# Kernel tuning notes

Hardware: AMD Instinct MI355X
Metric: run time of the kernel (lower is better)

Reference implementation:

```python
import jax, jax.numpy as jnp
import numpy as np

B, N, C = 2, 1024, 256
HEADS, DH = 8, 32
INNER = HEADS * DH
L, P = 3, 9
FF = 512
DEPTH = 2
KNN_K = (16, 64)
SHAPES_NP = np.array([[128, 128], [64, 64], [32, 32]], np.int32)
LEN = int((SHAPES_NP[:, 0] * SHAPES_NP[:, 1]).sum())


def _ln(x, g, b, eps=1e-5):
    m = x.mean(-1, keepdims=True)
    v = ((x - m) ** 2).mean(-1, keepdims=True)
    return (x - m) * jax.lax.rsqrt(v + eps) * g + b


def _knn_gather(x, pos, k):
    # pos: [B,N,3]; self-KNN (includes self as nearest)
    sq = jnp.sum(pos ** 2, -1)
    d2 = sq[:, :, None] + sq[:, None, :] - 2.0 * jnp.einsum('bnd,bmd->bnm', pos, pos)
    _, idx = jax.lax.top_k(-d2, k)  # [B,N,k]
    return jax.vmap(lambda xb, ib: xb[ib])(x, idx)  # [B,N,k,C]


def _self_attn_knn(x, pos3d, Wq, Wkv, Wo, bo, k):
    Bq, Nq, _ = x.shape
    knn_x = _knn_gather(x, pos3d, k)
    q = (x @ Wq).reshape(Bq, Nq, HEADS, DH)
    kk, vv = jnp.split(knn_x @ Wkv, 2, -1)
    kk = kk.reshape(Bq, Nq, k, HEADS, DH)
    vv = vv.reshape(Bq, Nq, k, HEADS, DH)
    attn = jax.nn.softmax(jnp.einsum('bnhd,bnshd->bnhs', q, kk) * (DH ** -0.5), -1)
    out = jnp.einsum('bnhs,bnshd->bnhd', attn, vv).reshape(Bq, Nq, INNER)
    return out @ Wo + bo


def _bilinear(value_l, loc, Hl, Wl):
    # value_l: [B, Hl*Wl, HEADS, DH]; loc: [B,N,HEADS,P,2] normalized [0,1]
    # grid_sample(align_corners=False, padding_mode='zeros') semantics
    Bq, Nq, Hh, Pp, _ = loc.shape
    xf = loc[..., 0] * Wl - 0.5
    yf = loc[..., 1] * Hl - 0.5
    x0 = jnp.floor(xf)
    y0 = jnp.floor(yf)
    out = jnp.zeros((Bq, Nq, Hh, Pp, DH), value_l.dtype)
    for dy in (0.0, 1.0):
        for dx in (0.0, 1.0):
            ix, iy = x0 + dx, y0 + dy
            w = (1.0 - jnp.abs(xf - ix)) * (1.0 - jnp.abs(yf - iy))
            valid = (ix >= 0) & (ix <= Wl - 1) & (iy >= 0) & (iy <= Hl - 1)
            flat = (jnp.clip(iy, 0, Hl - 1) * Wl + jnp.clip(ix, 0, Wl - 1)).astype(jnp.int32)
            flat = flat.transpose(0, 1, 3, 2).reshape(Bq, Nq * Pp, Hh)
            idx = jnp.broadcast_to(flat[..., None], (Bq, Nq * Pp, Hh, DH))
            g = jnp.take_along_axis(value_l, idx, axis=1)
            g = g.reshape(Bq, Nq, Pp, Hh, DH).transpose(0, 1, 3, 2, 4)
            out = out + g * (w * valid)[..., None]
    return out


def _msdeform(q, ref, value_src, Wval, bval, Woff, boff, Waw, baw, Wo, bo):
    Bq, Nq, _ = q.shape
    value = (value_src @ Wval + bval).reshape(Bq, -1, HEADS, DH)
    off = (q @ Woff + boff).reshape(Bq, Nq, HEADS, L, P, 2)
    aw = jax.nn.softmax((q @ Waw + baw).reshape(Bq, Nq, HEADS, L * P), -1)
    aw = aw.reshape(Bq, Nq, HEADS, L, P)
    normalizer = jnp.asarray(SHAPES_NP[:, ::-1].copy(), jnp.float32)  # (W,H) per level
    loc = ref[:, :, None, :, None, :] + off / normalizer[None, None, None, :, None, :]
    out = jnp.zeros((Bq, Nq, HEADS, DH), q.dtype)
    start = 0
    for l in range(L):
        Hl, Wl = int(SHAPES_NP[l, 0]), int(SHAPES_NP[l, 1])
        v_l = value[:, start:start + Hl * Wl]
        samp = _bilinear(v_l, loc[:, :, :, l], Hl, Wl)  # [B,N,H,P,DH]
        out = out + jnp.einsum('bnhpd,bnhp->bnhd', samp, aw[:, :, :, l])
        start += Hl * Wl
    return out.reshape(Bq, Nq, INNER) @ Wo + bo


def _forward(x, src, center_pos, center_pos3d, W_pos, b_pos, ln1_g, ln1_b, ln2_g, ln2_b, ln3_g, ln3_b,
             Wq, Wkv, Wo_sa, bo_sa, Wval, bval, Woff, boff, Waw, baw, Wo_ca, bo_ca, W1, b1, W2, b2):
    cpe = center_pos[..., 0, :] @ W_pos + b_pos  # pos_embedding(center_pos[...,0,:])
    ref = center_pos  # [B,N,L,2]
    for i in range(DEPTH):
        h = _ln(x + cpe, ln1_g[i], ln1_b[i])
        x = x + _self_attn_knn(h, center_pos3d, Wq[i], Wkv[i], Wo_sa[i], bo_sa[i], KNN_K[i])
        q = _ln(x, ln2_g[i], ln2_b[i]) + cpe  # with_pos_embed(norm(x), query_pos)
        s = _ln(src, ln2_g[i], ln2_b[i])      # PreNorm applies same LN to src
        x = x + _msdeform(q, ref, s, Wval[i], bval[i], Woff[i], boff[i], Waw[i], baw[i], Wo_ca[i], bo_ca[i])
        hf = _ln(x, ln3_g[i], ln3_b[i])
        x = x + (jax.nn.gelu(hf @ W1[i] + b1[i], approximate=False) @ W2[i] + b2[i])
    return x


def setup_inputs():
    key = jax.random.key(0)
    ks = iter(jax.random.split(key, 64))
    rn = lambda shape, s=1.0: jax.random.normal(next(ks), shape, jnp.float32) * s
    w = 0.02
    starts = np.concatenate([[0], np.cumsum(SHAPES_NP[:, 0] * SHAPES_NP[:, 1])[:-1]]).astype(np.int32)
    return {
        'x': rn((B, N, C)),
        'src': rn((B, LEN, C)),
        'center_pos': jax.random.uniform(next(ks), (B, N, L, 2), jnp.float32),
        'center_pos3d': rn((B, N, 3)),
        'spatial_shapes': jnp.asarray(SHAPES_NP),
        'level_start_index': jnp.asarray(starts),
        'W_pos': rn((2, C), w), 'b_pos': jnp.zeros((C,), jnp.float32),
        'ln1_g': jnp.ones((DEPTH, C)), 'ln1_b': jnp.zeros((DEPTH, C)),
        'ln2_g': jnp.ones((DEPTH, C)), 'ln2_b': jnp.zeros((DEPTH, C)),
        'ln3_g': jnp.ones((DEPTH, C)), 'ln3_b': jnp.zeros((DEPTH, C)),
        'Wq': rn((DEPTH, C, INNER), w), 'Wkv': rn((DEPTH, C, 2 * INNER), w),
        'Wo_sa': rn((DEPTH, INNER, C), w), 'bo_sa': jnp.zeros((DEPTH, C)),
        'Wval': rn((DEPTH, C, INNER), w), 'bval': jnp.zeros((DEPTH, INNER)),
        'Woff': rn((DEPTH, C, HEADS * L * P * 2), w), 'boff': rn((DEPTH, HEADS * L * P * 2), w),
        'Waw': rn((DEPTH, C, HEADS * L * P), w), 'baw': jnp.zeros((DEPTH, HEADS * L * P)),
        'Wo_ca': rn((DEPTH, INNER, C), w), 'bo_ca': jnp.zeros((DEPTH, C)),
        'W1': rn((DEPTH, C, FF), w), 'b1': jnp.zeros((DEPTH, FF)),
        'W2': rn((DEPTH, FF, C), w), 'b2': jnp.zeros((DEPTH, C)),
    }


def reference(x, src, center_pos, center_pos3d, spatial_shapes, level_start_index, W_pos, b_pos,
              ln1_g, ln1_b, ln2_g, ln2_b, ln3_g, ln3_b, Wq, Wkv, Wo_sa, bo_sa,
              Wval, bval, Woff, boff, Waw, baw, Wo_ca, bo_ca, W1, b1, W2, b2):
    # spatial_shapes / level_start_index are fixed constants (SHAPES_NP) baked into the level loop.
    return _forward(x, src, center_pos, center_pos3d, W_pos, b_pos, ln1_g, ln1_b, ln2_g, ln2_b,
                    ln3_g, ln3_b, Wq, Wkv, Wo_sa, bo_sa, Wval, bval, Woff, boff, Waw, baw,
                    Wo_ca, bo_ca, W1, b1, W2, b2)
```

## Files before the change

kernel.cpp:

```cpp
#include <hip/hip_runtime.h>
#include <math.h>


#define DEV __device__ __forceinline__

typedef __attribute__((ext_vector_type(8))) short bf16x8;
typedef __attribute__((ext_vector_type(4))) float floatx4;

DEV float gelu_f(float v) { return 0.5f * v * (1.0f + erff(v * 0.7071067811865475f)); }

DEV unsigned short f2bf(float f) {
    unsigned u = __float_as_uint(f);
    return (unsigned short)((u + 0x7fffu + ((u >> 16) & 1u)) >> 16);
}

__global__ __launch_bounds__(256) void k_lnsrc(const float* __restrict__ x, unsigned short* __restrict__ out) {
    int wid = threadIdx.x >> 6, lane = threadIdx.x & 63;
    size_t row = (size_t)blockIdx.x * 4 + wid;
    float4 v = ((const float4*)(x + row * 256))[lane];
    float s = (v.x + v.y) + (v.z + v.w);
#pragma unroll
    for (int o = 32; o; o >>= 1) s += __shfl_xor(s, o);
    float mean = s * (1.0f / 256.0f);
    float dx = v.x - mean, dy = v.y - mean, dz = v.z - mean, dw = v.w - mean;
    float q = (dx * dx + dy * dy) + (dz * dz + dw * dw);
#pragma unroll
    for (int o = 32; o; o >>= 1) q += __shfl_xor(q, o);
    float rstd = 1.0f / sqrtf(q * (1.0f / 256.0f) + 1e-5f);
    ushort4 o4;
    o4.x = f2bf(dx * rstd);
    o4.y = f2bf(dy * rstd);
    o4.z = f2bf(dz * rstd);
    o4.w = f2bf(dw * rstd);
    ((ushort4*)(out + row * 256))[lane] = o4;
}

__global__ __launch_bounds__(256) void k_lnfused(const float* __restrict__ x, const float* pre, const float* post,
                                                 const float* __restrict__ g, const float* __restrict__ b,
                                                 unsigned short* __restrict__ out) {
    int wid = threadIdx.x >> 6, lane = threadIdx.x & 63;
    size_t row = (size_t)blockIdx.x * 4 + wid;
    float4 v = ((const float4*)(x + row * 256))[lane];
    if (pre) {
        float4 p = ((const float4*)(pre + row * 256))[lane];
        v.x += p.x; v.y += p.y; v.z += p.z; v.w += p.w;
    }
    float s = (v.x + v.y) + (v.z + v.w);
#pragma unroll
    for (int o = 32; o; o >>= 1) s += __shfl_xor(s, o);
    float mean = s * (1.0f / 256.0f);
    float dx = v.x - mean, dy = v.y - mean, dz = v.z - mean, dw = v.w - mean;
    float q = (dx * dx + dy * dy) + (dz * dz + dw * dw);
#pragma unroll
    for (int o = 32; o; o >>= 1) q += __shfl_xor(q, o);
    float rstd = 1.0f / sqrtf(q * (1.0f / 256.0f) + 1e-5f);
    float4 gg = ((const float4*)g)[lane], bb = ((const float4*)b)[lane];
    float4 o4;
    o4.x = dx * rstd * gg.x + bb.x;
    o4.y = dy * rstd * gg.y + bb.y;
    o4.z = dz * rstd * gg.z + bb.z;
    o4.w = dw * rstd * gg.w + bb.w;
    if (post) {
        float4 p = ((const float4*)(post + row * 256))[lane];
        o4.x += p.x; o4.y += p.y; o4.z += p.z; o4.w += p.w;
    }
    ushort4 u4;
    u4.x = f2bf(o4.x); u4.y = f2bf(o4.y); u4.z = f2bf(o4.z); u4.w = f2bf(o4.w);
    ((ushort4*)(out + row * 256))[lane] = u4;
}

__global__ __launch_bounds__(256) void k_cpe(const float* __restrict__ cpos, const float* __restrict__ Wp,
                                             const float* __restrict__ bp, float* __restrict__ cpe) {
    int bn = blockIdx.x, c = threadIdx.x;
    float px = cpos[(size_t)bn * 6 + 0], py = cpos[(size_t)bn * 6 + 1];
    cpe[(size_t)bn * 256 + c] = px * Wp[c] + py * Wp[256 + c] + bp[c];
}

__global__ __launch_bounds__(256) void k_knn2(const float* __restrict__ pos, int* __restrict__ k16,
                                              int* __restrict__ k64) {
    __shared__ float sp[3072];
    int b = blockIdx.x >> 8;
    int n0 = (blockIdx.x & 255) * 4;
    for (int t = threadIdx.x; t < 3072; t += 256) sp[t] = pos[(size_t)b * 3072 + t];
    __syncthreads();
    int wid = threadIdx.x >> 6, lane = threadIdx.x & 63;
    int n = n0 + wid;
    float qx = sp[n * 3], qy = sp[n * 3 + 1], qz = sp[n * 3 + 2];
    float sqn = (qx * qx + qy * qy) + qz * qz;
    unsigned du[16];
#pragma unroll
    for (int t = 0; t < 16; t++) {
        int m = t * 64 + lane;
        float mx = sp[m * 3], my = sp[m * 3 + 1], mz = sp[m * 3 + 2];
        float sqm = (mx * mx + my * my) + mz * mz;
        float dt = (qx * mx + qy * my) + qz * mz;
        float d2 = (sqn + sqm) - 2.0f * dt;
        unsigned u = __float_as_uint(d2);
        du[t] = (u & 0x80000000u) ? ~u : (u | 0x80000000u);
    }
    unsigned long long lmask = (1ull << lane) - 1ull;

    auto cnt_le = [&](unsigned p) {
        int c = 0;
#pragma unroll
        for (int t = 0; t < 16; t++) c += __popcll(__ballot(du[t] <= p));
        return c;
    };
    auto find_T = [&](int K) {
        unsigned lo = 0u, hi = 0xFFFFFFFFu;
        while (lo < hi) {
            unsigned mid = lo + ((hi - lo) >> 1);
            if (cnt_le(mid) >= K) hi = mid; else lo = mid + 1;
        }
        return hi;
    };
    auto emit = [&](int K, unsigned T, int* out) {
        int base = 0;
#pragma unroll
        for (int t = 0; t < 16; t++) {
            bool lt = du[t] < T;
            unsigned long long mk = __ballot(lt);
            if (lt) out[base + __popcll(mk & lmask)] = t * 64 + lane;
            base += __popcll(mk);
        }
        int need = K - base, eb = 0;
#pragma unroll
        for (int t = 0; t < 16; t++) {
            bool eq = du[t] == T;
            unsigned long long mk = __ballot(eq);
            if (eq) {
                int r = eb + __popcll(mk & lmask);
                if (r < need) out[base + r] = t * 64 + lane;
            }
            eb += __popcll(mk);
        }
    };
    unsigned T16 = find_T(16);
    emit(16, T16, k16 + ((size_t)b * 1024 + n) * 16);
    unsigned T64 = find_T(64);
    emit(64, T64, k64 + ((size_t)b * 1024 + n) * 64);
}

template <int KK>
__global__ __launch_bounds__(256) void k_attn(const float* __restrict__ hqkv, const int* __restrict__ kidx,
                                              unsigned short* __restrict__ out) {
    int bn = blockIdx.x;
    int b = bn >> 10;
    int tid = threadIdx.x;
    __shared__ float sq[256];
    __shared__ float sa[8][KK];
    __shared__ int si[KK];
    if (tid < KK) si[tid] = kidx[(size_t)bn * KK + tid];
    sq[tid] = hqkv[(size_t)bn * 768 + tid] * 0.17677669529663689f;
    __syncthreads();
    const float* kvb = hqkv + (size_t)b * 1024 * 768;
#pragma unroll
    for (int pair = tid; pair < 8 * KK; pair += 256) {
        int s = pair & (KK - 1);
        int h = pair / KK;
        const float4* kr = (const float4*)(kvb + (size_t)si[s] * 768 + 256 + h * 32);
        const float4* q4 = (const float4*)&sq[h * 32];
        float a0 = 0.f, a1 = 0.f, a2 = 0.f, a3 = 0.f;
#pragma unroll
        for (int e = 0; e < 8; e++) {
            float4 kv = kr[e];
            float4 qv = q4[e];
            a0 = fmaf(kv.x, qv.x, a0);
            a1 = fmaf(kv.y, qv.y, a1);
            a2 = fmaf(kv.z, qv.z, a2);
            a3 = fmaf(kv.w, qv.w, a3);
        }
        sa[h][s] = (a0 + a1) + (a2 + a3);
    }
    __syncthreads();
    int h = tid >> 5, d = tid & 31;
    float mx = -1e30f;
    for (int s = d; s < KK; s += 32) mx = fmaxf(mx, sa[h][s]);
#pragma unroll
    for (int o = 16; o; o >>= 1) mx = fmaxf(mx, __shfl_xor(mx, o, 32));
    float sum = 0.0f;
    for (int s = d; s < KK; s += 32) {
        float e = __expf(sa[h][s] - mx);
        sa[h][s] = e;
        sum += e;
    }
#pragma unroll
    for (int o = 16; o; o >>= 1) sum += __shfl_xor(sum, o, 32);
    float inv = 1.0f / sum;
    __syncthreads();
    float acc = 0.0f;
    for (int s = 0; s < KK; s++) {
        float vv = kvb[(size_t)si[s] * 768 + 512 + tid];
        acc += sa[h][s] * vv;
    }
    out[(size_t)bn * 256 + tid] = f2bf(acc * inv);
}

__global__ __launch_bounds__(256) void k_msdeform(const float* __restrict__ offaw, const float* __restrict__ cpos,
                                                  const unsigned short* __restrict__ value_d,
                                                  unsigned short* __restrict__ out) {
    int bn = blockIdx.x;
    int b = bn >> 10;
    int tid = threadIdx.x;
    __shared__ float aw[216];
    __shared__ uint2 meta[864];
    __shared__ float sacc[2][256];
    if (tid < 216) aw[tid] = offaw[(size_t)bn * 648 + 432 + tid];
    __syncthreads();
    if (tid < 8) {
        float mx = -1e30f;
        for (int p = 0; p < 27; p++) mx = fmaxf(mx, aw[tid * 27 + p]);
        float s = 0.0f;
        for (int p = 0; p < 27; p++) {
            float e = __expf(aw[tid * 27 + p] - mx);
            aw[tid * 27 + p] = e;
            s += e;
        }
        float inv = 1.0f / s;
        for (int p = 0; p < 27; p++) aw[tid * 27 + p] *= inv;
    }
    __syncthreads();
    if (tid < 216) {
        int h = tid / 27, lp = tid - h * 27;
        int l = lp / 9;
        const int dims[3] = {128, 64, 32};
        const int starts[3] = {0, 16384, 20480};
        int Wl = dims[l], st = starts[l];
        float rx = cpos[(size_t)bn * 6 + l * 2], ry = cpos[(size_t)bn * 6 + l * 2 + 1];
        float ox = offaw[(size_t)bn * 648 + h * 54 + lp * 2];
        float oy = offaw[(size_t)bn * 648 + h * 54 + lp * 2 + 1];
        float rw = 1.0f / (float)Wl;
        float xf = (rx + ox * rw) * (float)Wl - 0.5f;
        float yf = (ry + oy * rw) * (float)Wl - 0.5f;
        float x0 = floorf(xf), y0 = floorf(yf);
        float wgt = aw[tid];
#pragma unroll
        for (int c = 0; c < 4; c++) {
            float ix = x0 + (float)(c & 1), iy = y0 + (float)(c >> 1);
            float w = (1.0f - fabsf(xf - ix)) * (1.0f - fabsf(yf - iy));
            bool valid = (ix >= 0.0f) & (ix <= (float)(Wl - 1)) & (iy >= 0.0f) & (iy <= (float)(Wl - 1));
            uint2 m;
            if (valid && w != 0.0f) {
                m.x = __float_as_uint(w * wgt);
                m.y = (unsigned)((st + (int)iy * Wl + (int)ix) * 1024);
            } else {
                m.x = 0u;
                m.y = 0u;
            }
            meta[tid * 4 + c] = m;
        }
    }
    __syncthreads();
    int par = tid >> 7, h2 = (tid >> 4) & 7, d2 = tid & 15;
    const char* base = (const char*)(value_d + (size_t)b * 21504 * 512) + h2 * 64 + d2 * 4;
    const uint2* mp = &meta[h2 * 108 + par * 54];
    float a0 = 0.f, a1 = 0.f;
#pragma unroll
    for (int j = 0; j < 54; j++) {
        uint2 m = mp[j];
        unsigned v = *(const unsigned*)(base + m.y);
        float w = __uint_as_float(m.x);
        a0 = fmaf(w, __uint_as_float(v << 16), a0);
        a1 = fmaf(w, __uint_as_float(v & 0xffff0000u), a1);
    }
    int ch = h2 * 32 + d2 * 2;
    sacc[par][ch] = a0;
    sacc[par][ch + 1] = a1;
    __syncthreads();
    out[(size_t)bn * 256 + tid] = f2bf(sacc[0][tid] + sacc[1][tid]);
}

struct TJobs {
    const float* src[18];
    const float* gam[18];
    unsigned short* dst[18];
    int K[18];
    int N[18];
};
__global__ __launch_bounds__(256) void k_tw(TJobs j) {
    int job = blockIdx.z;
    int K = j.K[job], N = j.N[job];
    int nt = (N + 31) >> 5, kt = K >> 5;
    if ((int)blockIdx.x >= nt || (int)blockIdx.y >= kt) return;
    __shared__ float t[32][33];
    const float* W = j.src[job];
    const float* g = j.gam[job];
    unsigned short* Wt = j.dst[job];
    int x = threadIdx.x & 31, y = threadIdx.x >> 5;
    int n0 = blockIdx.x << 5, k0 = blockIdx.y << 5;
#pragma unroll
    for (int i = 0; i < 32; i += 8) {
        int n = n0 + x;
        t[y + i][x] = (n < N) ? W[(size_t)(k0 + y + i) * N + n] : 0.0f;
    }
    __syncthreads();
    float gv = g ? g[k0 + x] : 1.0f;
#pragma unroll
    for (int i = 0; i < 32; i += 8) {
        int n = n0 + y + i;
        if (n < N) Wt[(size_t)n * K + k0 + x] = f2bf(gv * t[x][y + i]);
    }
}

__global__ __launch_bounds__(256) void k_foldval(const float* __restrict__ ln2b, const float* __restrict__ Wval,
                                                 const float* __restrict__ bval, float* __restrict__ out) {
    int d = blockIdx.x, n = threadIdx.x;
    const float* W = Wval + (size_t)d * 65536 + n;
    const float* lb = ln2b + d * 256;
    float s = bval[d * 256 + n];
    for (int k = 0; k < 256; k++) s = fmaf(lb[k], W[(size_t)k * 256], s);
    out[d * 256 + n] = s;
}

template <int BN, int WGM, int WGN, bool BIAS, bool BIAS2, bool GELUF, bool RES, bool OBF16>
__global__ __launch_bounds__(256) void k_mgemm(const unsigned short* __restrict__ A,
                                               const unsigned short* __restrict__ Bt,
                                               const float* __restrict__ bias, const float* __restrict__ bias2,
                                               int bsplit, const float* __restrict__ res, void* __restrict__ Cout,
                                               int M, int K, int Ncol) {
    constexpr int BM = 64, BK = 32;
    constexpr int WAVE_M = BM / WGM, WAVE_N = BN / WGN;
    constexpr int FM = WAVE_M / 16, FN = WAVE_N / 16;
    constexpr int BUN = BN / 64;
    __shared__ __align__(16) short a_lds[4][BM][8];
    __shared__ __align__(16) short b_lds[4][BN][8];
    int tid = threadIdx.x;
    int am0 = blockIdx.y * BM, bn0 = blockIdx.x * BN;
    int ar = tid >> 2, akc = tid & 3;
    const unsigned short* Arow = A + (size_t)(am0 + ar) * K + akc * 8;
    int4 aq;
    int4 bq[BUN];
    int nsteps = K / BK;

    auto load_tile = [&](int k0) {
        aq = *(const int4*)(Arow + k0);
#pragma unroll
        for (int jj = 0; jj < BUN; jj++) {
            int u = tid + 256 * jj;
            int col = u >> 2, kc = u & 3;
            int gn = bn0 + col;
            if (gn < Ncol)
                bq[jj] = *(const int4*)(Bt + (size_t)gn * K + k0 + kc * 8);
            else
                bq[jj] = make_int4(0, 0, 0, 0);
        }
    };
    auto write_lds = [&]() {
        *(int4*)(&a_lds[akc][ar ^ akc][0]) = aq;
#pragma unroll
        for (int jj = 0; jj < BUN; jj++) {
            int u = tid + 256 * jj;
            int col = u >> 2, kc = u & 3;
            *(int4*)(&b_lds[kc][col ^ kc][0]) = bq[jj];
        }
    };
    int lane = tid & 63, wid = tid >> 6;
    int wm = wid / WGN, wn = wid % WGN;
    int fr = lane & 15, fkc = lane >> 4;
    floatx4 acc[FM][FN] = {};

    load_tile(0);
    for (int t = 0; t < nsteps; ++t) {
        if (t) __syncthreads();
        write_lds();
        __syncthreads();
        if (t + 1 < nsteps) load_tile((t + 1) * BK);
        bf16x8 af[FM], bf[FN];
#pragma unroll
        for (int m = 0; m < FM; m++) af[m] = *(const bf16x8*)(&a_lds[fkc][(wm * WAVE_M + m * 16 + fr) ^ fkc][0]);
#pragma unroll
        for (int n = 0; n < FN; n++) bf[n] = *(const bf16x8*)(&b_lds[fkc][(wn * WAVE_N + n * 16 + fr) ^ fkc][0]);
#pragma unroll
        for (int m = 0; m < FM; m++)
#pragma unroll
            for (int n = 0; n < FN; n++)
                acc[m][n] = __builtin_amdgcn_mfma_f32_16x16x32_bf16(af[m], bf[n], acc[m][n], 0, 0, 0);
    }
    int r4 = lane >> 4;
#pragma unroll
    for (int m = 0; m < FM; m++) {
        int row = am0 + wm * WAVE_M + m * 16 + r4 * 4;
#pragma unroll
        for (int n = 0; n < FN; n++) {
            int col = bn0 + wn * WAVE_N + n * 16 + fr;
            if (col < Ncol) {
                float bsc = 0.0f;
                if (BIAS) bsc = (BIAS2 && col >= bsplit) ? bias2[col - bsplit] : bias[col];
#pragma unroll
                for (int r = 0; r < 4; r++) {
                    size_t off = (size_t)(row + r) * Ncol + col;
                    float v = acc[m][n][r] + bsc;
                    if (GELUF) v = gelu_f(v);
                    if (RES) v += res[off];
                    if (OBF16)
                        ((unsigned short*)Cout)[off] = f2bf(v);
                    else
                        ((float*)Cout)[off] = v;
                }
            }
        }
    }
}

extern "C" void kernel_launch(void* const* d_in, const int* in_sizes, int n_in, void* d_out, int out_size,
                              void* d_ws, size_t ws_size, hipStream_t stream) {
    const float* xin = (const float*)d_in[0];
    const float* src = (const float*)d_in[1];
    const float* cpos = (const float*)d_in[2];
    const float* pos3 = (const float*)d_in[3];
    const float* Wpos = (const float*)d_in[6];
    const float* bpos = (const float*)d_in[7];
    const float* ln1g = (const float*)d_in[8];
    const float* ln1b = (const float*)d_in[9];
    const float* ln2g = (const float*)d_in[10];
    const float* ln2b = (const float*)d_in[11];
    const float* ln3g = (const float*)d_in[12];
    const float* ln3b = (const float*)d_in[13];
    const float* Wq = (const float*)d_in[14];
    const float* Wkv = (const float*)d_in[15];
    const float* Wosa = (const float*)d_in[16];
    const float* bosa = (const float*)d_in[17];
    const float* Wval = (const float*)d_in[18];
    const float* bval = (const float*)d_in[19];
    const float* Woff = (const float*)d_in[20];
    const float* boff = (const float*)d_in[21];
    const float* Waw = (const float*)d_in[22];
    const float* baw = (const float*)d_in[23];
    const float* Woca = (const float*)d_in[24];
    const float* boca = (const float*)d_in[25];
    const float* W1 = (const float*)d_in[26];
    const float* b1f = (const float*)d_in[27];
    const float* W2 = (const float*)d_in[28];
    const float* b2f = (const float*)d_in[29];
    float* x = (float*)d_out;

    float* ws = (float*)d_ws;
    float* cpe = ws;
    float* hqkv = cpe + 524288;
    float* offaw = hqkv + 1572864;
    float* bval2 = offaw + 1327104;
    unsigned short* lnout16 = (unsigned short*)(bval2 + 512);
    unsigned short* attn16 = lnout16 + 524288;
    unsigned short* cab16 = attn16 + 524288;
    unsigned short* ffmid16 = cab16 + 524288;
    unsigned short* srcn16 = ffmid16 + 1048576;
    unsigned short* value16 = srcn16 + 11010048;
    int* kidx16 = (int*)(value16 + 22020096);
    int* kidx64 = kidx16 + 32768;
    unsigned short* wt = (unsigned short*)(kidx64 + 131072);

    const size_t WT_STRIDE = 755712;
    const size_t O_WQKV = 0, O_WOSA = 196608, O_WOFFAW = 262144, O_WOCA = 428032,
                 O_W1 = 493568, O_W2 = 624640;
    unsigned short* wtval = wt + 2 * WT_STRIDE;

    TJobs tj;
    for (int d = 0; d < 2; d++) {
        unsigned short* wd = wt + (size_t)d * WT_STRIDE;
        int tb = d * 9;
        tj.src[tb + 0] = Wq + (size_t)d * 65536;    tj.gam[tb + 0] = nullptr;      tj.dst[tb + 0] = wd + O_WQKV;            tj.K[tb + 0] = 256; tj.N[tb + 0] = 256;
        tj.src[tb + 1] = Wkv + (size_t)d * 131072;  tj.gam[tb + 1] = nullptr;      tj.dst[tb + 1] = wd + O_WQKV + 65536;    tj.K[tb + 1] = 256; tj.N[tb + 1] = 512;
        tj.src[tb + 2] = Wosa + (size_t)d * 65536;  tj.gam[tb + 2] = nullptr;      tj.dst[tb + 2] = wd + O_WOSA;            tj.K[tb + 2] = 256; tj.N[tb + 2] = 256;
        tj.src[tb + 3] = Woff + (size_t)d * 110592; tj.gam[tb + 3] = nullptr;      tj.dst[tb + 3] = wd + O_WOFFAW;          tj.K[tb + 3] = 256; tj.N[tb + 3] = 432;
        tj.src[tb + 4] = Waw + (size_t)d * 55296;   tj.gam[tb + 4] = nullptr;      tj.dst[tb + 4] = wd + O_WOFFAW + 110592; tj.K[tb + 4] = 256; tj.N[tb + 4] = 216;
        tj.src[tb + 5] = Woca + (size_t)d * 65536;  tj.gam[tb + 5] = nullptr;      tj.dst[tb + 5] = wd + O_WOCA;            tj.K[tb + 5] = 256; tj.N[tb + 5] = 256;
        tj.src[tb + 6] = W1 + (size_t)d * 131072;   tj.gam[tb + 6] = nullptr;      tj.dst[tb + 6] = wd + O_W1;              tj.K[tb + 6] = 256; tj.N[tb + 6] = 512;
        tj.src[tb + 7] = W2 + (size_t)d * 131072;   tj.gam[tb + 7] = nullptr;      tj.dst[tb + 7] = wd + O_W2;              tj.K[tb + 7] = 512; tj.N[tb + 7] = 256;
        tj.src[tb + 8] = Wval + (size_t)d * 65536;  tj.gam[tb + 8] = ln2g + d * 256; tj.dst[tb + 8] = wtval + (size_t)d * 65536; tj.K[tb + 8] = 256; tj.N[tb + 8] = 256;
    }
    k_tw<<<dim3(16, 16, 18), 256, 0, stream>>>(tj);
    k_foldval<<<2, 256, 0, stream>>>(ln2b, Wval, bval, bval2);

    k_cpe<<<2048, 256, 0, stream>>>(cpos, Wpos, bpos, cpe);
    k_lnsrc<<<10752, 256, 0, stream>>>(src, srcn16);
    k_knn2<<<512, 256, 0, stream>>>(pos3, kidx16, kidx64);

    k_mgemm<256, 1, 4, true, false, false, false, true><<<dim3(2, 672), 256, 0, stream>>>(
        srcn16, wtval, bval2, nullptr, 0, nullptr, value16, 43008, 256, 512);

    for (int i = 0; i < 2; i++) {
        unsigned short* wd = wt + (size_t)i * WT_STRIDE;
        const float* xc = (i == 0) ? xin : x;
        k_lnfused<<<512, 256, 0, stream>>>(xc, cpe, nullptr, ln1g + i * 256, ln1b + i * 256, lnout16);
        k_mgemm<64, 2, 2, false, false, false, false, false><<<dim3(12, 32), 256, 0, stream>>>(
            lnout16, wd + O_WQKV, nullptr, nullptr, 0, nullptr, hqkv, 2048, 256, 768);
        if (i == 0)
            k_attn<16><<<2048, 256, 0, stream>>>(hqkv, kidx16, attn16);
        else
            k_attn<64><<<2048, 256, 0, stream>>>(hqkv, kidx64, attn16);
        k_mgemm<64, 2, 2, true, false, false, true, false><<<dim3(4, 32), 256, 0, stream>>>(
            attn16, wd + O_WOSA, bosa + i * 256, nullptr, 0, xc, x, 2048, 256, 256);

        k_lnfused<<<512, 256, 0, stream>>>(x, nullptr, cpe, ln2g + i * 256, ln2b + i * 256, lnout16);
        k_mgemm<64, 2, 2, true, true, false, false, false><<<dim3(11, 32), 256, 0, stream>>>(
            lnout16, wd + O_WOFFAW, boff + i * 432, baw + i * 216, 432, nullptr, offaw, 2048, 256, 648);
        k_msdeform<<<2048, 256, 0, stream>>>(offaw, cpos, value16 + (size_t)i * 256, cab16);
        k_mgemm<64, 2, 2, true, false, false, true, false><<<dim3(4, 32), 256, 0, stream>>>(
            cab16, wd + O_WOCA, boca + i * 256, nullptr, 0, x, x, 2048, 256, 256);

        k_lnfused<<<512, 256, 0, stream>>>(x, nullptr, nullptr, ln3g + i * 256, ln3b + i * 256, lnout16);
        k_mgemm<64, 2, 2, true, false, true, false, true><<<dim3(8, 32), 256, 0, stream>>>(
            lnout16, wd + O_W1, b1f + i * 512, nullptr, 0, nullptr, ffmid16, 2048, 256, 512);
        k_mgemm<64, 2, 2, true, false, false, true, false><<<dim3(4, 32), 256, 0, stream>>>(
            ffmid16, wd + O_W2, b2f + i * 256, nullptr, 0, x, x, 2048, 512, 256);
    }
}
```

Measured before the change: 237.8 us.

## Add full-K single-load GEMM for K=256 layers and merge foldval into cpe

Adds k_fgemm, which loads the entire 64x256 A and B tiles into swizzled LDS once, synchronizes a single time, and then runs all MFMA steps. It replaces the per-K-step pipelined k_mgemm for every K=256 GEMM in the decoder loop, removing the repeated LDS barriers that dominate small GEMMs. The bias fold kernel is merged into the cpe kernel as two extra blocks, saving one launch. The cost is 64KB of LDS per block, which may limit occupancy.

```diff
diff --git a/kernel.cpp b/kernel.cpp
--- a/kernel.cpp
+++ b/kernel.cpp
@@ -69,11 +69,22 @@
     ((ushort4*)(out + row * 256))[lane] = u4;
 }
 
-__global__ __launch_bounds__(256) void k_cpe(const float* __restrict__ cpos, const float* __restrict__ Wp,
-                                             const float* __restrict__ bp, float* __restrict__ cpe) {
-    int bn = blockIdx.x, c = threadIdx.x;
-    float px = cpos[(size_t)bn * 6 + 0], py = cpos[(size_t)bn * 6 + 1];
-    cpe[(size_t)bn * 256 + c] = px * Wp[c] + py * Wp[256 + c] + bp[c];
+__global__ __launch_bounds__(256) void k_cpe2(const float* __restrict__ cpos, const float* __restrict__ Wp,
+                                              const float* __restrict__ bp, float* __restrict__ cpe,
+                                              const float* __restrict__ ln2b, const float* __restrict__ Wval,
+                                              const float* __restrict__ bval, float* __restrict__ bval2) {
+    if (blockIdx.x < 2048) {
+        int bn = blockIdx.x, c = threadIdx.x;
+        float px = cpos[(size_t)bn * 6 + 0], py = cpos[(size_t)bn * 6 + 1];
+        cpe[(size_t)bn * 256 + c] = px * Wp[c] + py * Wp[256 + c] + bp[c];
+    } else {
+        int d = blockIdx.x - 2048, n = threadIdx.x;
+        const float* W = Wval + (size_t)d * 65536 + n;
+        const float* lb = ln2b + d * 256;
+        float s = bval[d * 256 + n];
+        for (int k = 0; k < 256; k++) s = fmaf(lb[k], W[(size_t)k * 256], s);
+        bval2[d * 256 + n] = s;
+    }
 }
 
 __global__ __launch_bounds__(256) void k_knn2(const float* __restrict__ pos, int* __restrict__ k16,
@@ -302,22 +313,88 @@
     }
 }
 
-__global__ __launch_bounds__(256) void k_foldval(const float* __restrict__ ln2b, const float* __restrict__ Wval,
-                                                 const float* __restrict__ bval, float* __restrict__ out) {
-    int d = blockIdx.x, n = threadIdx.x;
-    const float* W = Wval + (size_t)d * 65536 + n;
-    const float* lb = ln2b + d * 256;
-    float s = bval[d * 256 + n];
-    for (int k = 0; k < 256; k++) s = fmaf(lb[k], W[(size_t)k * 256], s);
-    out[d * 256 + n] = s;
-}
-
-template <int BN, int WGM, int WGN, bool BIAS, bool BIAS2, bool GELUF, bool RES, bool OBF16>
-__global__ __launch_bounds__(256) void k_mgemm(const unsigned short* __restrict__ A,
+template <bool BIAS, bool BIAS2, bool GELUF, bool RES, bool OBF16>
+__global__ __launch_bounds__(256) void k_fgemm(const unsigned short* __restrict__ A,
                                                const unsigned short* __restrict__ Bt,
                                                const float* __restrict__ bias, const float* __restrict__ bias2,
                                                int bsplit, const float* __restrict__ res, void* __restrict__ Cout,
-                                               int M, int K, int Ncol) {
+                                               int Ncol) {
+    constexpr int K = 256, CH = 32;
+    __shared__ int4 a_lds[64 * CH];
+    __shared__ int4 b_lds[64 * CH];
+    int tid = threadIdx.x;
+    int am0 = blockIdx.y * 64, bn0 = blockIdx.x * 64;
+    int kc = tid & (CH - 1), rg = (tid / CH) * 8;
+    const int4* Ag = (const int4*)(A + (size_t)(am0 + rg) * K) + kc;
+#pragma unroll
+    for (int j = 0; j < 8; j++) {
+        int row = rg + j;
+        a_lds[row * CH + (kc ^ (row & 31))] = Ag[(size_t)j * CH];
+    }
+#pragma unroll
+    for (int j = 0; j < 8; j++) {
+        int row = rg + j;
+        int n = bn0 + row;
+        int4 v = make_int4(0, 0, 0, 0);
+        if (n < Ncol) v = *((const int4*)(Bt + (size_t)n * K) + kc);
+        b_lds[row * CH + (kc ^ (row & 31))] = v;
+    }
+    __syncthreads();
+    int lane = tid & 63, wid = tid >> 6;
+    int wm = wid >> 1, wn = wid & 1;
+    int fr = lane & 15, fkc = lane >> 4;
+    floatx4 acc[2][2] = {};
+#pragma unroll
+    for (int s = 0; s < 8; s++) {
+        int kk = s * 4 + fkc;
+        bf16x8 af[2], bf[2];
+#pragma unroll
+        for (int m = 0; m < 2; m++) {
+            int row = wm * 32 + m * 16 + fr;
+            af[m] = *(const bf16x8*)&a_lds[row * CH + (kk ^ (row & 31))];
+        }
+#pragma unroll
+        for (int n = 0; n < 2; n++) {
+            int row = wn * 32 + n * 16 + fr;
+            bf[n] = *(const bf16x8*)&b_lds[row * CH + (kk ^ (row & 31))];
+        }
+#pragma unroll
+        for (int m = 0; m < 2; m++)
+#pragma unroll
+            for (int n = 0; n < 2; n++)
+                acc[m][n] = __builtin_amdgcn_mfma_f32_16x16x32_bf16(af[m], bf[n], acc[m][n], 0, 0, 0);
+    }
+    int r4 = lane >> 4;
+#pragma unroll
+    for (int m = 0; m < 2; m++) {
+        int row = am0 + wm * 32 + m * 16 + r4 * 4;
+#pragma unroll
+        for (int n = 0; n < 2; n++) {
+            int col = bn0 + wn * 32 + n * 16 + fr;
+            if (col < Ncol) {
+                float bsc = 0.0f;
+                if (BIAS) bsc = (BIAS2 && col >= bsplit) ? bias2[col - bsplit] : bias[col];
+#pragma unroll
+                for (int r = 0; r < 4; r++) {
+                    size_t off = (size_t)(row + r) * Ncol + col;
+                    float v = acc[m][n][r] + bsc;
+                    if (GELUF) v = gelu_f(v);
+                    if (RES) v += res[off];
+                    if (OBF16)
+                        ((unsigned short*)Cout)[off] = f2bf(v);
+                    else
+                        ((float*)Cout)[off] = v;
+                }
+            }
+        }
+    }
+}
+
+template <int BN, int WGM, int WGN, bool BIAS, bool GELUF, bool RES, bool OBF16>
+__global__ __launch_bounds__(256) void k_mgemm(const unsigned short* __restrict__ A,
+                                               const unsigned short* __restrict__ Bt,
+                                               const float* __restrict__ bias, const float* __restrict__ res,
+                                               void* __restrict__ Cout, int M, int K, int Ncol) {
     constexpr int BM = 64, BK = 32;
     constexpr int WAVE_M = BM / WGM, WAVE_N = BN / WGN;
     constexpr int FM = WAVE_M / 16, FN = WAVE_N / 16;
@@ -384,8 +461,7 @@
         for (int n = 0; n < FN; n++) {
             int col = bn0 + wn * WAVE_N + n * 16 + fr;
             if (col < Ncol) {
-                float bsc = 0.0f;
-                if (BIAS) bsc = (BIAS2 && col >= bsplit) ? bias2[col - bsplit] : bias[col];
+                float bsc = BIAS ? bias[col] : 0.0f;
 #pragma unroll
                 for (int r = 0; r < 4; r++) {
                     size_t off = (size_t)(row + r) * Ncol + col;
@@ -469,39 +545,38 @@
         tj.src[tb + 8] = Wval + (size_t)d * 65536;  tj.gam[tb + 8] = ln2g + d * 256; tj.dst[tb + 8] = wtval + (size_t)d * 65536; tj.K[tb + 8] = 256; tj.N[tb + 8] = 256;
     }
     k_tw<<<dim3(16, 16, 18), 256, 0, stream>>>(tj);
-    k_foldval<<<2, 256, 0, stream>>>(ln2b, Wval, bval, bval2);
-
-    k_cpe<<<2048, 256, 0, stream>>>(cpos, Wpos, bpos, cpe);
+    k_cpe2<<<2050, 256, 0, stream>>>(cpos, Wpos, bpos, cpe, ln2b, Wval, bval, bval2);
+
     k_lnsrc<<<10752, 256, 0, stream>>>(src, srcn16);
     k_knn2<<<512, 256, 0, stream>>>(pos3, kidx16, kidx64);
 
-    k_mgemm<256, 1, 4, true, false, false, false, true><<<dim3(2, 672), 256, 0, stream>>>(
-        srcn16, wtval, bval2, nullptr, 0, nullptr, value16, 43008, 256, 512);
+    k_mgemm<256, 1, 4, true, false, false, true><<<dim3(2, 672), 256, 0, stream>>>(
+        srcn16, wtval, bval2, nullptr, value16, 43008, 256, 512);
 
     for (int i = 0; i < 2; i++) {
         unsigned short* wd = wt + (size_t)i * WT_STRIDE;
         const float* xc = (i == 0) ? xin : x;
         k_lnfused<<<512, 256, 0, stream>>>(xc, cpe, nullptr, ln1g + i * 256, ln1b + i * 256, lnout16);
-        k_mgemm<64, 2, 2, false, false, false, false, false><<<dim3(12, 32), 256, 0, stream>>>(
-            lnout16, wd + O_WQKV, nullptr, nullptr, 0, nullptr, hqkv, 2048, 256, 768);
+        k_fgemm<false, false, false, false, false><<<dim3(12, 32), 256, 0, stream>>>(
+            lnout16, wd + O_WQKV, nullptr, nullptr, 0, nullptr, hqkv, 768);
         if (i == 0)
             k_attn<16><<<2048, 256, 0, stream>>>(hqkv, kidx16, attn16);
         else
             k_attn<64><<<2048, 256, 0, stream>>>(hqkv, kidx64, attn16);
-        k_mgemm<64, 2, 2, true, false, false, true, false><<<dim3(4, 32), 256, 0, stream>>>(
-            attn16, wd + O_WOSA, bosa + i * 256, nullptr, 0, xc, x, 2048, 256, 256);
+        k_fgemm<true, false, false, true, false><<<dim3(4, 32), 256, 0, stream>>>(
+            attn16, wd + O_WOSA, bosa + i * 256, nullptr, 0, xc, x, 256);
 
         k_lnfused<<<512, 256, 0, stream>>>(x, nullptr, cpe, ln2g + i * 256, ln2b + i * 256, lnout16);
-        k_mgemm<64, 2, 2, true, true, false, false, false><<<dim3(11, 32), 256, 0, stream>>>(
-            lnout16, wd + O_WOFFAW, boff + i * 432, baw + i * 216, 432, nullptr, offaw, 2048, 256, 648);
+        k_fgemm<true, true, false, false, false><<<dim3(11, 32), 256, 0, stream>>>(
+            lnout16, wd + O_WOFFAW, boff + i * 432, baw + i * 216, 432, nullptr, offaw, 648);
         k_msdeform<<<2048, 256, 0, stream>>>(offaw, cpos, value16 + (size_t)i * 256, cab16);
-        k_mgemm<64, 2, 2, true, false, false, true, false><<<dim3(4, 32), 256, 0, stream>>>(
-            cab16, wd + O_WOCA, boca + i * 256, nullptr, 0, x, x, 2048, 256, 256);
+        k_fgemm<true, false, false, true, false><<<dim3(4, 32), 256, 0, stream>>>(
+            cab16, wd + O_WOCA, boca + i * 256, nullptr, 0, x, x, 256);
 
         k_lnfused<<<512, 256, 0, stream>>>(x, nullptr, nullptr, ln3g + i * 256, ln3b + i * 256, lnout16);
-        k_mgemm<64, 2, 2, true, false, true, false, true><<<dim3(8, 32), 256, 0, stream>>>(
-            lnout16, wd + O_W1, b1f + i * 512, nullptr, 0, nullptr, ffmid16, 2048, 256, 512);
-        k_mgemm<64, 2, 2, true, false, false, true, false><<<dim3(4, 32), 256, 0, stream>>>(
-            ffmid16, wd + O_W2, b2f + i * 256, nullptr, 0, x, x, 2048, 512, 256);
-    }
-}
+        k_fgemm<true, false, true, false, true><<<dim3(8, 32), 256, 0, stream>>>(
+            lnout16, wd + O_W1, b1f + i * 512, nullptr, 0, nullptr, ffmid16, 512);
+        k_mgemm<64, 2, 2, true, false, true, false><<<dim3(4, 32), 256, 0, stream>>>(
+            ffmid16, wd + O_W2, b2f + i * 256, x, x, 2048, 512, 256);
+    }
+}
```

New measurement: 246.2 us. +3.5%, slower.

## Stage GEMM tiles with direct global-to-LDS loads and double buffering

Applied to the files above, without the earlier changes.

The bf16 MFMA GEMM now stages A and B tiles with the global_load_lds builtin, which writes straight into LDS instead of going through registers. It uses two LDS buffers so the next K-step is fetched while the current one is computed, with one barrier per step. The XOR swizzle and the Ncol bounds guard on B loads are dropped, which risks LDS bank conflicts and out-of-range B row reads when Ncol is not a multiple of BN. Separately, the bias-folding kernel is merged into the positional-embedding kernel to save one launch.

```diff
diff --git a/kernel.cpp b/kernel.cpp
--- a/kernel.cpp
+++ b/kernel.cpp
@@ -12,6 +12,11 @@
 DEV unsigned short f2bf(float f) {
     unsigned u = __float_as_uint(f);
     return (unsigned short)((u + 0x7fffu + ((u >> 16) & 1u)) >> 16);
+}
+
+DEV void gload_lds16(const unsigned short* g, short* l) {
+    __builtin_amdgcn_global_load_lds((const __attribute__((address_space(1))) void*)g,
+                                     (__attribute__((address_space(3))) void*)l, 16, 0, 0);
 }
 
 __global__ __launch_bounds__(256) void k_lnsrc(const float* __restrict__ x, unsigned short* __restrict__ out) {
@@ -69,11 +74,22 @@
     ((ushort4*)(out + row * 256))[lane] = u4;
 }
 
-__global__ __launch_bounds__(256) void k_cpe(const float* __restrict__ cpos, const float* __restrict__ Wp,
-                                             const float* __restrict__ bp, float* __restrict__ cpe) {
-    int bn = blockIdx.x, c = threadIdx.x;
-    float px = cpos[(size_t)bn * 6 + 0], py = cpos[(size_t)bn * 6 + 1];
-    cpe[(size_t)bn * 256 + c] = px * Wp[c] + py * Wp[256 + c] + bp[c];
+__global__ __launch_bounds__(256) void k_cpe2(const float* __restrict__ cpos, const float* __restrict__ Wp,
+                                              const float* __restrict__ bp, float* __restrict__ cpe,
+                                              const float* __restrict__ ln2b, const float* __restrict__ Wval,
+                                              const float* __restrict__ bval, float* __restrict__ bval2) {
+    if (blockIdx.x < 2048) {
+        int bn = blockIdx.x, c = threadIdx.x;
+        float px = cpos[(size_t)bn * 6 + 0], py = cpos[(size_t)bn * 6 + 1];
+        cpe[(size_t)bn * 256 + c] = px * Wp[c] + py * Wp[256 + c] + bp[c];
+    } else {
+        int d = blockIdx.x - 2048, n = threadIdx.x;
+        const float* W = Wval + (size_t)d * 65536 + n;
+        const float* lb = ln2b + d * 256;
+        float s = bval[d * 256 + n];
+        for (int k = 0; k < 256; k++) s = fmaf(lb[k], W[(size_t)k * 256], s);
+        bval2[d * 256 + n] = s;
+    }
 }
 
 __global__ __launch_bounds__(256) void k_knn2(const float* __restrict__ pos, int* __restrict__ k16,
@@ -302,18 +318,8 @@
     }
 }
 
-__global__ __launch_bounds__(256) void k_foldval(const float* __restrict__ ln2b, const float* __restrict__ Wval,
-                                                 const float* __restrict__ bval, float* __restrict__ out) {
-    int d = blockIdx.x, n = threadIdx.x;
-    const float* W = Wval + (size_t)d * 65536 + n;
-    const float* lb = ln2b + d * 256;
-    float s = bval[d * 256 + n];
-    for (int k = 0; k < 256; k++) s = fmaf(lb[k], W[(size_t)k * 256], s);
-    out[d * 256 + n] = s;
-}
-
 template <int BN, int WGM, int WGN, bool BIAS, bool BIAS2, bool GELUF, bool RES, bool OBF16>
-__global__ __launch_bounds__(256) void k_mgemm(const unsigned short* __restrict__ A,
+__global__ __launch_bounds__(256) void k_ggemm(const unsigned short* __restrict__ A,
                                                const unsigned short* __restrict__ Bt,
                                                const float* __restrict__ bias, const float* __restrict__ bias2,
                                                int bsplit, const float* __restrict__ res, void* __restrict__ Cout,
@@ -322,59 +328,42 @@
     constexpr int WAVE_M = BM / WGM, WAVE_N = BN / WGN;
     constexpr int FM = WAVE_M / 16, FN = WAVE_N / 16;
     constexpr int BUN = BN / 64;
-    __shared__ __align__(16) short a_lds[4][BM][8];
-    __shared__ __align__(16) short b_lds[4][BN][8];
+    __shared__ __align__(16) short a_lds[2][4][BM][8];
+    __shared__ __align__(16) short b_lds[2][4][BN][8];
     int tid = threadIdx.x;
+    int lane = tid & 63, w = tid >> 6;
     int am0 = blockIdx.y * BM, bn0 = blockIdx.x * BN;
-    int ar = tid >> 2, akc = tid & 3;
-    const unsigned short* Arow = A + (size_t)(am0 + ar) * K + akc * 8;
-    int4 aq;
-    int4 bq[BUN];
-    int nsteps = K / BK;
-
-    auto load_tile = [&](int k0) {
-        aq = *(const int4*)(Arow + k0);
-#pragma unroll
-        for (int jj = 0; jj < BUN; jj++) {
-            int u = tid + 256 * jj;
-            int col = u >> 2, kc = u & 3;
-            int gn = bn0 + col;
-            if (gn < Ncol)
-                bq[jj] = *(const int4*)(Bt + (size_t)gn * K + k0 + kc * 8);
-            else
-                bq[jj] = make_int4(0, 0, 0, 0);
-        }
+    const unsigned short* Asrc = A + (size_t)(am0 + lane) * K + w * 8;
+    const unsigned short* Bsrc = Bt + (size_t)(bn0 + lane) * K + w * 8;
+
+    auto stage = [&](int k0, int buf) {
+        gload_lds16(Asrc + k0, &a_lds[buf][w][0][0]);
+#pragma unroll
+        for (int j = 0; j < BUN; j++)
+            gload_lds16(Bsrc + (size_t)j * 64 * K + k0, &b_lds[buf][w][j * 64][0]);
     };
-    auto write_lds = [&]() {
-        *(int4*)(&a_lds[akc][ar ^ akc][0]) = aq;
-#pragma unroll
-        for (int jj = 0; jj < BUN; jj++) {
-            int u = tid + 256 * jj;
-            int col = u >> 2, kc = u & 3;
-            *(int4*)(&b_lds[kc][col ^ kc][0]) = bq[jj];
-        }
-    };
-    int lane = tid & 63, wid = tid >> 6;
-    int wm = wid / WGN, wn = wid % WGN;
+
+    int wm = w / WGN, wn = w % WGN;
     int fr = lane & 15, fkc = lane >> 4;
     floatx4 acc[FM][FN] = {};
-
-    load_tile(0);
+    int nsteps = K / BK;
+
+    stage(0, 0);
+    int buf = 0;
     for (int t = 0; t < nsteps; ++t) {
-        if (t) __syncthreads();
-        write_lds();
         __syncthreads();
-        if (t + 1 < nsteps) load_tile((t + 1) * BK);
+        if (t + 1 < nsteps) stage((t + 1) * BK, buf ^ 1);
         bf16x8 af[FM], bf[FN];
 #pragma unroll
-        for (int m = 0; m < FM; m++) af[m] = *(const bf16x8*)(&a_lds[fkc][(wm * WAVE_M + m * 16 + fr) ^ fkc][0]);
-#pragma unroll
-        for (int n = 0; n < FN; n++) bf[n] = *(const bf16x8*)(&b_lds[fkc][(wn * WAVE_N + n * 16 + fr) ^ fkc][0]);
+        for (int m = 0; m < FM; m++) af[m] = *(const bf16x8*)(&a_lds[buf][fkc][wm * WAVE_M + m * 16 + fr][0]);
+#pragma unroll
+        for (int n = 0; n < FN; n++) bf[n] = *(const bf16x8*)(&b_lds[buf][fkc][wn * WAVE_N + n * 16 + fr][0]);
 #pragma unroll
         for (int m = 0; m < FM; m++)
 #pragma unroll
             for (int n = 0; n < FN; n++)
                 acc[m][n] = __builtin_amdgcn_mfma_f32_16x16x32_bf16(af[m], bf[n], acc[m][n], 0, 0, 0);
+        buf ^= 1;
     }
     int r4 = lane >> 4;
 #pragma unroll
@@ -469,39 +458,38 @@
         tj.src[tb + 8] = Wval + (size_t)d * 65536;  tj.gam[tb + 8] = ln2g + d * 256; tj.dst[tb + 8] = wtval + (size_t)d * 65536; tj.K[tb + 8] = 256; tj.N[tb + 8] = 256;
     }
     k_tw<<<dim3(16, 16, 18), 256, 0, stream>>>(tj);
-    k_foldval<<<2, 256, 0, stream>>>(ln2b, Wval, bval, bval2);
-
-    k_cpe<<<2048, 256, 0, stream>>>(cpos, Wpos, bpos, cpe);
+    k_cpe2<<<2050, 256, 0, stream>>>(cpos, Wpos, bpos, cpe, ln2b, Wval, bval, bval2);
+
     k_lnsrc<<<10752, 256, 0, stream>>>(src, srcn16);
     k_knn2<<<512, 256, 0, stream>>>(pos3, kidx16, kidx64);
 
-    k_mgemm<256, 1, 4, true, false, false, false, true><<<dim3(2, 672), 256, 0, stream>>>(
+    k_ggemm<256, 1, 4, true, false, false, false, true><<<dim3(2, 672), 256, 0, stream>>>(
         srcn16, wtval, bval2, nullptr, 0, nullptr, value16, 43008, 256, 512);
 
     for (int i = 0; i < 2; i++) {
         unsigned short* wd = wt + (size_t)i * WT_STRIDE;
         const float* xc = (i == 0) ? xin : x;
         k_lnfused<<<512, 256, 0, stream>>>(xc, cpe, nullptr, ln1g + i * 256, ln1b + i * 256, lnout16);
-        k_mgemm<64, 2, 2, false, false, false, false, false><<<dim3(12, 32), 256, 0, stream>>>(
+        k_ggemm<64, 2, 2, false, false, false, false, false><<<dim3(12, 32), 256, 0, stream>>>(
             lnout16, wd + O_WQKV, nullptr, nullptr, 0, nullptr, hqkv, 2048, 256, 768);
         if (i == 0)
             k_attn<16><<<2048, 256, 0, stream>>>(hqkv, kidx16, attn16);
         else
             k_attn<64><<<2048, 256, 0, stream>>>(hqkv, kidx64, attn16);
-        k_mgemm<64, 2, 2, true, false, false, true, false><<<dim3(4, 32), 256, 0, stream>>>(
+        k_ggemm<64, 2, 2, true, false, false, true, false><<<dim3(4, 32), 256, 0, stream>>>(
             attn16, wd + O_WOSA, bosa + i * 256, nullptr, 0, xc, x, 2048, 256, 256);
 
         k_lnfused<<<512, 256, 0, stream>>>(x, nullptr, cpe, ln2g + i * 256, ln2b + i * 256, lnout16);
-        k_mgemm<64, 2, 2, true, true, false, false, false><<<dim3(11, 32), 256, 0, stream>>>(
+        k_ggemm<64, 2, 2, true, true, false, false, false><<<dim3(11, 32), 256, 0, stream>>>(
             lnout16, wd + O_WOFFAW, boff + i * 432, baw + i * 216, 432, nullptr, offaw, 2048, 256, 648);
         k_msdeform<<<2048, 256, 0, stream>>>(offaw, cpos, value16 + (size_t)i * 256, cab16);
-        k_mgemm<64, 2, 2, true, false, false, true, false><<<dim3(4, 32), 256, 0, stream>>>(
+        k_ggemm<64, 2, 2, true, false, false, true, false><<<dim3(4, 32), 256, 0, stream>>>(
             cab16, wd + O_WOCA, boca + i * 256, nullptr, 0, x, x, 2048, 256, 256);
 
         k_lnfused<<<512, 256, 0, stream>>>(x, nullptr, nullptr, ln3g + i * 256, ln3b + i * 256, lnout16);
-        k_mgemm<64, 2, 2, true, false, true, false, true><<<dim3(8, 32), 256, 0, stream>>>(
+        k_ggemm<64, 2, 2, true, false, true, false, true><<<dim3(8, 32), 256, 0, stream>>>(
             lnout16, wd + O_W1, b1f + i * 512, nullptr, 0, nullptr, ffmid16, 2048, 256, 512);
-        k_mgemm<64, 2, 2, true, false, false, true, false><<<dim3(4, 32), 256, 0, stream>>>(
+        k_ggemm<64, 2, 2, true, false, false, true, false><<<dim3(4, 32), 256, 0, stream>>>(
             ffmid16, wd + O_W2, b2f + i * 256, nullptr, 0, x, x, 2048, 512, 256);
     }
 }
```

New measurement: 268.8 us. +13.0%, slower.
